# Optimization experiments

Measured on AMD Instinct MI355X. Metric: run time of the kernel, lower is better.

Reference implementation:

```python
import jax, jax.numpy as jnp
import numpy as np

N = 50000      # nodes
E = 800000     # raw edges (self-loops added inside reference, PyG GATConv default)
H = 8          # attention heads
DH = 16        # head dim
HID = H * DH   # 128 hidden
L = 4          # num GAT layers
G = 16         # graphs in the batch
EPS = 1e-5
NEG_SLOPE = 0.2


def setup_inputs() -> dict:
    key = jax.random.key(0)
    ks = jax.random.split(key, 8)
    s = 0.05
    x = jax.random.normal(ks[0], (N, 64), jnp.float32)
    edge_index = jax.random.randint(ks[1], (2, E), 0, N, dtype=jnp.int32).astype(jnp.int64)
    batch = jnp.sort(jax.random.randint(ks[2], (N,), 0, G, dtype=jnp.int32)).astype(jnp.int64)
    in_W = jax.random.normal(ks[3], (64, HID), jnp.float32) * s
    in_b = jnp.zeros((HID,), jnp.float32)
    Wg = jax.random.normal(ks[4], (L, HID, HID), jnp.float32) * s
    att_src = jax.random.normal(ks[5], (L, H, DH), jnp.float32) * s
    att_dst = jax.random.normal(ks[6], (L, H, DH), jnp.float32) * s
    gat_b = jnp.zeros((L, HID), jnp.float32)
    gn_w = jnp.ones((L, HID), jnp.float32)
    gn_b = jnp.zeros((L, HID), jnp.float32)
    gn_s = jnp.ones((L, HID), jnp.float32)  # GraphNorm mean_scale
    return {"x": x, "edge_index": edge_index, "batch": batch, "in_W": in_W,
            "in_b": in_b, "Wg": Wg, "att_src": att_src, "att_dst": att_dst,
            "gat_b": gat_b, "gn_w": gn_w, "gn_b": gn_b, "gn_s": gn_s}


def _gat_conv(h_in, src, dst, W, a_src, a_dst, bias):
    # PyG GATConv: per-head linear, additive attention, softmax over incoming edges
    h = (h_in @ W).reshape(N, H, DH)                       # [N,H,DH]
    e_src = jnp.sum(h * a_src, axis=-1)                    # [N,H]
    e_dst = jnp.sum(h * a_dst, axis=-1)                    # [N,H]
    e = jax.nn.leaky_relu(e_src[src] + e_dst[dst], NEG_SLOPE)  # [E',H]
    m = jax.ops.segment_max(e, dst, num_segments=N)        # per-dst max (stable softmax)
    m = jnp.where(jnp.isfinite(m), m, 0.0)
    ex = jnp.exp(e - m[dst])
    denom = jax.ops.segment_sum(ex, dst, num_segments=N)
    alpha = ex / (denom[dst] + 1e-16)                      # [E',H]
    msg = h[src] * alpha[..., None]                        # [E',H,DH]
    out = jax.ops.segment_sum(msg, dst, num_segments=N)    # [N,H,DH]
    return out.reshape(N, HID) + bias


def _graph_norm(x, batch, w, b, scale):
    cnt = jax.ops.segment_sum(jnp.ones((N, 1), x.dtype), batch, num_segments=G)
    mean = jax.ops.segment_sum(x, batch, num_segments=G) / cnt        # [G,HID]
    out = x - scale * mean[batch]
    var = jax.ops.segment_sum(out * out, batch, num_segments=G) / cnt # [G,HID]
    return out / jnp.sqrt(var + EPS)[batch] * w + b


def reference(x, edge_index, batch, in_W, in_b, Wg, att_src, att_dst, gat_b, gn_w, gn_b, gn_s):
    # add self-loops (PyG GATConv default add_self_loops=True)
    loop = jnp.arange(N, dtype=edge_index.dtype)
    src = jnp.concatenate([edge_index[0], loop])
    dst = jnp.concatenate([edge_index[1], loop])
    h = x @ in_W + in_b                                    # input_proj -> [N,HID]
    for i in range(L):
        attn = _gat_conv(h, src, dst, Wg[i], att_src[i], att_dst[i], gat_b[i])
        h = attn + h                                       # identity residual (in==out)
        h = _graph_norm(h, batch, gn_w[i], gn_b[i], gn_s[i])
        # dropout is identity in eval mode
    return h
```

## Files before the change

### kernel.cpp

```cpp
#include <hip/hip_runtime.h>
#include <cstdint>
#include <cstddef>

#define Nn   50000
#define Ee   800000
#define ETOT 850000
#define HID  128
#define Gg   16
#define RSZ  6250
#define NEG_SLOPE 0.2f
#define EPS_GN 1e-5f

typedef __attribute__((ext_vector_type(8))) short short8;
typedef __attribute__((ext_vector_type(4))) float f32x4;

static __device__ __forceinline__ float lrelu(float v) { return v > 0.f ? v : NEG_SLOPE * v; }

static __device__ __forceinline__ unsigned int f2bf(float x) {
    unsigned int u = __float_as_uint(x);
    return (u + 0x7fffu + ((u >> 16) & 1u)) >> 16;
}
static __device__ __forceinline__ float bf_lo(unsigned int u) { return __uint_as_float(u << 16); }
static __device__ __forceinline__ float bf_hi(unsigned int u) { return __uint_as_float(u & 0xffff0000u); }

__global__ void prep_w(const float* __restrict__ in_W, const float* __restrict__ Wg,
                       short* __restrict__ Wt0, short* __restrict__ Wtl) {
    int i = blockIdx.x * 256 + threadIdx.x;
    if (i < 8192) {
        int n = i >> 6, k = i & 63;
        Wt0[i] = (short)f2bf(in_W[k * 128 + n]);
    } else if (i < 73728) {
        int j = i - 8192;
        int l = j >> 14;
        int rkn = j & 16383;
        int n = rkn >> 7, k = rkn & 127;
        Wtl[j] = (short)f2bf(Wg[l * 16384 + k * 128 + n]);
    }
}

__global__ void count_deg(const int* __restrict__ edst, int* __restrict__ deg) {
    int r  = blockIdx.x & 7;
    int cb = blockIdx.x >> 3;
    int nb = gridDim.x >> 3;
    int lo = r * RSZ, hi = lo + RSZ;
    for (int i = cb * 256 + threadIdx.x; i < ETOT; i += nb * 256) {
        int dst = (i < Ee) ? edst[i] : (i - Ee);
        if (dst >= lo && dst < hi) atomicAdd(&deg[dst], 1);
    }
}

__global__ void scatter_edges(const int* __restrict__ esrc, const int* __restrict__ edst,
                              int* __restrict__ cur, int* __restrict__ col) {
    int r  = blockIdx.x & 7;
    int cb = blockIdx.x >> 3;
    int nb = gridDim.x >> 3;
    int lo = r * RSZ, hi = lo + RSZ;
    for (int i = cb * 256 + threadIdx.x; i < ETOT; i += nb * 256) {
        int dst = (i < Ee) ? edst[i] : (i - Ee);
        if (dst >= lo && dst < hi) {
            int src = (i < Ee) ? esrc[i] : dst;
            int pos = atomicAdd(&cur[dst], 1);
            col[pos] = src;
        }
    }
}

__global__ __launch_bounds__(1024) void scan1(const int* __restrict__ deg,
                                              int* __restrict__ rowptr,
                                              int* __restrict__ bsums) {
    __shared__ int sm[1024];
    int tid = threadIdx.x;
    int i = blockIdx.x * 1024 + tid;
    sm[tid] = (i < Nn) ? deg[i] : 0;
    __syncthreads();
    for (int off = 1; off < 1024; off <<= 1) {
        int t = 0;
        if (tid >= off) t = sm[tid - off];
        __syncthreads();
        sm[tid] += t;
        __syncthreads();
    }
    if (i < Nn) rowptr[i + 1] = sm[tid];
    if (tid == 1023) bsums[blockIdx.x] = sm[1023];
}

__global__ void scan2(int* __restrict__ bsums, int nb) {
    if (threadIdx.x == 0 && blockIdx.x == 0) {
        int run = 0;
        for (int b = 0; b < nb; b++) { int t = bsums[b]; bsums[b] = run; run += t; }
    }
}

__global__ void scan3(int* __restrict__ rowptr, const int* __restrict__ bsums) {
    int i = blockIdx.x * 256 + threadIdx.x;
    if (i == 0) rowptr[0] = 0;
    if (i < Nn) rowptr[i + 1] += bsums[i >> 10];
}

template <int K, bool AFFINE, bool OUT_BF16, bool BIAS>
__global__ __launch_bounds__(256) void gemm_mfma(const float* __restrict__ Ag,
                                                 const int* __restrict__ batch,
                                                 const float* __restrict__ Ab,
                                                 const float* __restrict__ Bb,
                                                 const short* __restrict__ Wt,
                                                 const float* __restrict__ bias,
                                                 float* __restrict__ Cf,
                                                 unsigned int* __restrict__ Cb,
                                                 int M) {
    constexpr int KP = K + 8;
    constexpr int ABYTES = 128 * KP * 2;
    constexpr int CBYTES = OUT_BF16 ? 64 * 130 * 4 : 0;
    constexpr int SBYTES = ABYTES > CBYTES ? ABYTES : CBYTES;
    __shared__ __align__(16) char smem[SBYTES];
    short* As = (short*)smem;
    float* Cs = (float*)smem;

    int t    = threadIdx.x;
    int lane = t & 63;
    int w    = t >> 6;
    int wm   = (w & 1) * 64;
    int wn   = (w >> 1) * 64;
    int row0 = blockIdx.x * 128;

    constexpr int F4R = K / 4;
    constexpr int ITERS = 128 * F4R / 256;
#pragma unroll
    for (int i = 0; i < ITERS; i++) {
        int f4 = t + 256 * i;
        int r  = f4 / F4R;
        int c4 = f4 % F4R;
        float4 v = make_float4(0.f, 0.f, 0.f, 0.f);
        int gr = row0 + r;
        if (gr < M) {
            v = *(const float4*)(Ag + (size_t)gr * K + c4 * 4);
            if (AFFINE) {
                int g = batch[gr];
                float4 Av = *(const float4*)(Ab + g * 128 + c4 * 4);
                float4 Bv = *(const float4*)(Bb + g * 128 + c4 * 4);
                v.x = v.x * Av.x + Bv.x;
                v.y = v.y * Av.y + Bv.y;
                v.z = v.z * Av.z + Bv.z;
                v.w = v.w * Av.w + Bv.w;
            }
        }
        uint2 pk;
        pk.x = f2bf(v.x) | (f2bf(v.y) << 16);
        pk.y = f2bf(v.z) | (f2bf(v.w) << 16);
        *(uint2*)(As + r * KP + c4 * 4) = pk;
    }
    __syncthreads();

    f32x4 acc[4][4] = {};
    int am = wm + (lane & 15);
    int aq = (lane >> 4) * 8;
    const short* wb = Wt + (size_t)(wn + (lane & 15)) * K + aq;
#pragma unroll
    for (int kk = 0; kk < K / 32; kk++) {
        short8 a[4], b[4];
#pragma unroll
        for (int nt = 0; nt < 4; nt++)
            b[nt] = *(const short8*)(wb + nt * 16 * K + kk * 32);
#pragma unroll
        for (int mt = 0; mt < 4; mt++)
            a[mt] = *(const short8*)(As + (am + mt * 16) * KP + kk * 32 + aq);
#pragma unroll
        for (int mt = 0; mt < 4; mt++)
#pragma unroll
            for (int nt = 0; nt < 4; nt++)
                acc[mt][nt] = __builtin_amdgcn_mfma_f32_16x16x32_bf16(
                    a[mt], b[nt], acc[mt][nt], 0, 0, 0);
    }

    if (!OUT_BF16) {
        float bv[4] = {0.f, 0.f, 0.f, 0.f};
        if (BIAS) {
#pragma unroll
            for (int nt = 0; nt < 4; nt++) bv[nt] = bias[wn + nt * 16 + (lane & 15)];
        }
#pragma unroll
        for (int mt = 0; mt < 4; mt++) {
#pragma unroll
            for (int reg = 0; reg < 4; reg++) {
                int row = row0 + wm + mt * 16 + (lane >> 4) * 4 + reg;
                if (row >= M) continue;
#pragma unroll
                for (int nt = 0; nt < 4; nt++)
                    Cf[(size_t)row * 128 + wn + nt * 16 + (lane & 15)] =
                        acc[mt][nt][reg] + bv[nt];
            }
        }
    } else {
#pragma unroll
        for (int half = 0; half < 2; half++) {
            __syncthreads();
            if ((w & 1) == half) {
#pragma unroll
                for (int mt = 0; mt < 4; mt++)
#pragma unroll
                    for (int reg = 0; reg < 4; reg++) {
                        int lr = mt * 16 + (lane >> 4) * 4 + reg;
#pragma unroll
                        for (int nt = 0; nt < 4; nt++)
                            Cs[lr * 130 + wn + nt * 16 + (lane & 15)] = acc[mt][nt][reg];
                    }
            }
            __syncthreads();
#pragma unroll
            for (int i = 0; i < 4; i++) {
                int u4 = t + 256 * i;
                int r  = u4 >> 4;
                int cu = (u4 & 15) * 4;
                int grow = row0 + half * 64 + r;
                if (grow < M) {
                    const float* cp = Cs + r * 130 + cu * 2;
                    float2 p0 = *(const float2*)(cp + 0);
                    float2 p1 = *(const float2*)(cp + 2);
                    float2 p2 = *(const float2*)(cp + 4);
                    float2 p3 = *(const float2*)(cp + 6);
                    uint4 o;
                    o.x = f2bf(p0.x) | (f2bf(p0.y) << 16);
                    o.y = f2bf(p1.x) | (f2bf(p1.y) << 16);
                    o.z = f2bf(p2.x) | (f2bf(p2.y) << 16);
                    o.w = f2bf(p3.x) | (f2bf(p3.y) << 16);
                    *(uint4*)(Cb + (size_t)grow * 64 + cu) = o;
                }
            }
        }
    }
}

__global__ __launch_bounds__(256) void att_scores(const unsigned int* __restrict__ hp,
                                                  const float* __restrict__ asrc,
                                                  const float* __restrict__ adst,
                                                  float* __restrict__ es,
                                                  float* __restrict__ ed) {
    int i = blockIdx.x * 256 + threadIdx.x;
    if (i >= Nn * 8) return;
    int hh = i & 7;
    const uint4* p = (const uint4*)(hp + (size_t)(i >> 3) * 64 + hh * 8);
    uint4 q0 = p[0], q1 = p[1];
    unsigned int qq[8] = {q0.x, q0.y, q0.z, q0.w, q1.x, q1.y, q1.z, q1.w};
    const float* av = asrc + hh * 16;
    const float* dv = adst + hh * 16;
    float s1 = 0.f, s2 = 0.f;
#pragma unroll
    for (int q = 0; q < 8; q++) {
        float x0 = bf_lo(qq[q]), x1 = bf_hi(qq[q]);
        s1 += x0 * av[2 * q] + x1 * av[2 * q + 1];
        s2 += x0 * dv[2 * q] + x1 * dv[2 * q + 1];
    }
    es[i] = s1;
    ed[i] = s2;
}

template <bool AFF>
__global__ __launch_bounds__(256) void gat_attn(const unsigned int* __restrict__ hp,
                                                const float* hin,
                                                const int* __restrict__ batch,
                                                const float* __restrict__ Ab,
                                                const float* __restrict__ Bb,
                                                const float* __restrict__ es,
                                                const float* __restrict__ ed,
                                                const int* __restrict__ rowptr,
                                                const int* __restrict__ col,
                                                const float* __restrict__ gbias,
                                                float* out) {
    int w    = threadIdx.x >> 6;
    int lane = threadIdx.x & 63;
    int n    = blockIdx.x * 4 + w;
    int start = rowptr[n], end = rowptr[n + 1];

    int slot = lane >> 3;
    int ah   = lane & 7;
    int ch   = lane >> 3;

    float edh = ed[(size_t)n * 8 + ah];

    float2 acc = make_float2(0.f, 0.f);
    float dacc = 0.f;

    int e0 = start;
    for (; e0 + 8 <= end; e0 += 8) {
        int src_l = col[e0 + slot];
        float wgt = __expf(lrelu(es[(size_t)src_l * 8 + ah] + edh));
        dacc += wgt;
#pragma unroll
        for (int j = 0; j < 8; j++) {
            int   src_j = __shfl(src_l, j * 8);
            float wj    = __shfl(wgt,   j * 8 + ch);
            unsigned int hv = hp[(size_t)src_j * 64 + lane];
            acc.x += wj * bf_lo(hv);
            acc.y += wj * bf_hi(hv);
        }
    }
    if (e0 < end) {
        int rem = end - e0;
        int eb  = e0 + slot;
        int ec  = (slot < rem) ? eb : (end - 1);
        int src_l = col[ec];
        float wgt = (slot < rem) ? __expf(lrelu(es[(size_t)src_l * 8 + ah] + edh)) : 0.f;
        dacc += wgt;
        for (int j = 0; j < rem; j++) {
            int   src_j = __shfl(src_l, j * 8);
            float wj    = __shfl(wgt,   j * 8 + ch);
            unsigned int hv = hp[(size_t)src_j * 64 + lane];
            acc.x += wj * bf_lo(hv);
            acc.y += wj * bf_hi(hv);
        }
    }

    dacc += __shfl_xor(dacc, 8);
    dacc += __shfl_xor(dacc, 16);
    dacc += __shfl_xor(dacc, 32);
    float inv  = 1.0f / (dacc + 1e-16f);
    float winv = __shfl(inv, ch);

    size_t idx = (size_t)n * 128 + 2 * lane;
    float2 xv = *(const float2*)(hin + idx);
    float2 res;
    if (AFF) {
        int g = batch[n];
        float2 Av = *(const float2*)(Ab + g * 128 + 2 * lane);
        float2 Bv = *(const float2*)(Bb + g * 128 + 2 * lane);
        res.x = xv.x * Av.x + Bv.x;
        res.y = xv.y * Av.y + Bv.y;
    } else {
        res = xv;
    }
    float2 o;
    o.x = acc.x * winv + gbias[2 * lane]     + res.x;
    o.y = acc.y * winv + gbias[2 * lane + 1] + res.y;
    *(float2*)(out + idx) = o;
}

#define SCHUNK 64
__global__ __launch_bounds__(128) void gn_stats(const float* __restrict__ x,
                                                const int* __restrict__ batch,
                                                float* __restrict__ sumx,
                                                float* __restrict__ sumxx,
                                                float* __restrict__ cnt) {
    int c  = threadIdx.x;
    int n0 = blockIdx.x * SCHUNK;
    int n1 = n0 + SCHUNK;
    if (n1 > Nn) n1 = Nn;
    if (n0 >= Nn) return;
    int curG = batch[n0];
    float sx = 0.f, sxx = 0.f;
    int run = 0;
    for (int n = n0; n < n1; n++) {
        int g = batch[n];
        if (g != curG) {
            atomicAdd(&sumx[curG * 128 + c], sx);
            atomicAdd(&sumxx[curG * 128 + c], sxx);
            if (c == 0) atomicAdd(&cnt[curG], (float)run);
            sx = 0.f; sxx = 0.f; run = 0; curG = g;
        }
        float v = x[(size_t)n * 128 + c];
        sx += v; sxx += v * v; run++;
    }
    atomicAdd(&sumx[curG * 128 + c], sx);
    atomicAdd(&sumxx[curG * 128 + c], sxx);
    if (c == 0) atomicAdd(&cnt[curG], (float)run);
}

__global__ void gn_final(const float* __restrict__ sumx, const float* __restrict__ sumxx,
                         const float* __restrict__ cnt, const float* __restrict__ w,
                         const float* __restrict__ b, const float* __restrict__ s,
                         float* __restrict__ Ab, float* __restrict__ Bb) {
    int i = blockIdx.x * blockDim.x + threadIdx.x;
    if (i >= Gg * 128) return;
    int g = i >> 7, c = i & 127;
    float cn  = cnt[g];
    float m   = sumx[i] / cn;
    float msq = sumxx[i] / cn;
    float sc  = s[c];
    float varo = msq - (2.f * sc - sc * sc) * m * m;
    float inv  = rsqrtf(varo + EPS_GN);
    float Ai   = inv * w[c];
    Ab[i] = Ai;
    Bb[i] = b[c] - sc * m * Ai;
    (void)g;
}

__global__ __launch_bounds__(256) void gn_apply(const float* __restrict__ x,
                                                const int* __restrict__ batch,
                                                const float* __restrict__ Ab,
                                                const float* __restrict__ Bb,
                                                float* __restrict__ out) {
    int idx = blockIdx.x * 256 + threadIdx.x;
    int n = idx >> 5;
    if (n >= Nn) return;
    int c4 = (idx & 31) << 2;
    int g = batch[n];
    float4 xv = *(const float4*)(x + (size_t)n * 128 + c4);
    float4 Av = *(const float4*)(Ab + g * 128 + c4);
    float4 Bv = *(const float4*)(Bb + g * 128 + c4);
    float4 o;
    o.x = xv.x * Av.x + Bv.x;
    o.y = xv.y * Av.y + Bv.y;
    o.z = xv.z * Av.z + Bv.z;
    o.w = xv.w * Av.w + Bv.w;
    *(float4*)(out + (size_t)n * 128 + c4) = o;
}

extern "C" void kernel_launch(void* const* d_in, const int* in_sizes, int n_in,
                              void* d_out, int out_size, void* d_ws, size_t ws_size,
                              hipStream_t stream) {
    const float* x      = (const float*)d_in[0];
    const int*   eidx   = (const int*)d_in[1];
    const int*   batch  = (const int*)d_in[2];
    const float* in_W   = (const float*)d_in[3];
    const float* in_b   = (const float*)d_in[4];
    const float* Wg     = (const float*)d_in[5];
    const float* attS   = (const float*)d_in[6];
    const float* attD   = (const float*)d_in[7];
    const float* gat_b  = (const float*)d_in[8];
    const float* gn_w   = (const float*)d_in[9];
    const float* gn_b   = (const float*)d_in[10];
    const float* gn_s   = (const float*)d_in[11];

    const int* esrc = eidx;
    const int* edst = eidx + Ee;

    char* p = (char*)d_ws;
    auto carve = [&](size_t bytes) {
        void* r = (void*)p;
        p += (bytes + 255) & ~(size_t)255;
        return r;
    };
    float* h0   = (float*)carve((size_t)Nn * 128 * 4);
    unsigned int* hp = (unsigned int*)carve((size_t)Nn * 64 * 4);
    float* h2   = (float*)carve((size_t)Nn * 128 * 4);
    float* es   = (float*)carve((size_t)Nn * 8 * 4);
    float* ed   = (float*)carve((size_t)Nn * 8 * 4);
    float* sumx = (float*)carve((size_t)(Gg * 128 * 2 + 16) * 4);
    float* sumxx = sumx + Gg * 128;
    float* cntf  = sumx + Gg * 128 * 2;
    float* Abuf = (float*)carve((size_t)Gg * 128 * 4);
    float* Bbuf = (float*)carve((size_t)Gg * 128 * 4);
    int* rowptr = (int*)carve((size_t)(Nn + 1) * 4);
    int* deg    = (int*)carve((size_t)Nn * 4);
    int* cur    = (int*)carve((size_t)Nn * 4);
    int* col    = (int*)carve((size_t)ETOT * 4);
    int* bsums  = (int*)carve(64 * 4);
    short* Wt0  = (short*)carve((size_t)128 * 64 * 2);
    short* Wtl  = (short*)carve((size_t)4 * 128 * 128 * 2);

    prep_w<<<288, 256, 0, stream>>>(in_W, Wg, Wt0, Wtl);
    hipMemsetAsync(deg, 0, (size_t)Nn * 4, stream);
    count_deg<<<768, 256, 0, stream>>>(edst, deg);
    scan1<<<(Nn + 1023) / 1024, 1024, 0, stream>>>(deg, rowptr, bsums);
    scan2<<<1, 64, 0, stream>>>(bsums, (Nn + 1023) / 1024);
    scan3<<<(Nn + 255) / 256, 256, 0, stream>>>(rowptr, bsums);
    hipMemcpyAsync(cur, rowptr, (size_t)Nn * 4, hipMemcpyDeviceToDevice, stream);
    scatter_edges<<<768, 256, 0, stream>>>(esrc, edst, cur, col);

    const int gemm_grid = (Nn + 127) / 128;

    gemm_mfma<64, false, false, true><<<gemm_grid, 256, 0, stream>>>(
        x, nullptr, nullptr, nullptr, Wt0, in_b, h0, nullptr, Nn);

    for (int l = 0; l < 4; l++) {
        const short* Wl = Wtl + (size_t)l * 128 * 128;
        if (l == 0) {
            gemm_mfma<128, false, true, false><<<gemm_grid, 256, 0, stream>>>(
                h0, nullptr, nullptr, nullptr, Wl, nullptr, nullptr, hp, Nn);
        } else {
            gemm_mfma<128, true, true, false><<<gemm_grid, 256, 0, stream>>>(
                h2, batch, Abuf, Bbuf, Wl, nullptr, nullptr, hp, Nn);
        }
        att_scores<<<(Nn * 8 + 255) / 256, 256, 0, stream>>>(hp, attS + l * 128,
                                                             attD + l * 128, es, ed);
        if (l == 0) {
            gat_attn<false><<<Nn / 4, 256, 0, stream>>>(hp, h0, nullptr, nullptr, nullptr,
                                                        es, ed, rowptr, col,
                                                        gat_b + l * 128, h2);
        } else {
            gat_attn<true><<<Nn / 4, 256, 0, stream>>>(hp, h2, batch, Abuf, Bbuf,
                                                       es, ed, rowptr, col,
                                                       gat_b + l * 128, h2);
        }
        hipMemsetAsync(sumx, 0, (size_t)(Gg * 128 * 2 + 16) * 4, stream);
        gn_stats<<<(Nn + SCHUNK - 1) / SCHUNK, 128, 0, stream>>>(h2, batch, sumx, sumxx, cntf);
        gn_final<<<8, 256, 0, stream>>>(sumx, sumxx, cntf, gn_w + l * 128,
                                        gn_b + l * 128, gn_s + l * 128, Abuf, Bbuf);
    }
    gn_apply<<<(Nn * 32 + 255) / 256, 256, 0, stream>>>(h2, batch, Abuf, Bbuf,
                                                        (float*)d_out);
    (void)in_sizes; (void)n_in; (void)out_size; (void)ws_size;
}
```

Baseline: 598.3 us.

## Fuse attention scores into GEMM epilogue and widen per-lane gathers in gat_attn

Drops the separate att_scores kernel and computes the per-head source and destination attention dot products in the bf16 GEMM epilogue, from the fp32 tile already held in shared memory. The scores now come from unrounded fp32 values rather than bf16-rounded ones. The aggregation kernel now has each half-wave handle alternate edges and each lane load 4 bf16 values (uint2), with a cross-half reduction at the end. The separate tail loop is removed by masking invalid edges to zero weight. This saves one launch and one re-read of hp per layer, but costs extra shuffles and some idle lanes in the final store.

Measured after the change: 575.9 us. -3.8%, faster.

```diff
diff --git a/kernel.cpp b/kernel.cpp
--- a/kernel.cpp
+++ b/kernel.cpp
@@ -97,13 +97,17 @@
     if (i < Nn) rowptr[i + 1] += bsums[i >> 10];
 }
 
-template <int K, bool AFFINE, bool OUT_BF16, bool BIAS>
+template <int K, bool AFFINE, bool OUT_BF16, bool BIAS, bool SCORES>
 __global__ __launch_bounds__(256) void gemm_mfma(const float* __restrict__ Ag,
                                                  const int* __restrict__ batch,
                                                  const float* __restrict__ Ab,
                                                  const float* __restrict__ Bb,
                                                  const short* __restrict__ Wt,
                                                  const float* __restrict__ bias,
+                                                 const float* __restrict__ asrc,
+                                                 const float* __restrict__ adst,
+                                                 float* __restrict__ es,
+                                                 float* __restrict__ ed,
                                                  float* __restrict__ Cf,
                                                  unsigned int* __restrict__ Cb,
                                                  int M) {
@@ -190,6 +194,15 @@
             }
         }
     } else {
+        float avv[8], dvv[8];
+        if (SCORES) {
+            int q = t & 15;
+#pragma unroll
+            for (int k = 0; k < 8; k++) {
+                avv[k] = asrc[q * 8 + k];
+                dvv[k] = adst[q * 8 + k];
+            }
+        }
 #pragma unroll
         for (int half = 0; half < 2; half++) {
             __syncthreads();
@@ -223,34 +236,25 @@
                     o.z = f2bf(p2.x) | (f2bf(p2.y) << 16);
                     o.w = f2bf(p3.x) | (f2bf(p3.y) << 16);
                     *(uint4*)(Cb + (size_t)grow * 64 + cu) = o;
+                    if (SCORES) {
+                        float s1 = p0.x * avv[0] + p0.y * avv[1] + p1.x * avv[2] +
+                                   p1.y * avv[3] + p2.x * avv[4] + p2.y * avv[5] +
+                                   p3.x * avv[6] + p3.y * avv[7];
+                        float s2 = p0.x * dvv[0] + p0.y * dvv[1] + p1.x * dvv[2] +
+                                   p1.y * dvv[3] + p2.x * dvv[4] + p2.y * dvv[5] +
+                                   p3.x * dvv[6] + p3.y * dvv[7];
+                        s1 += __shfl_xor(s1, 1);
+                        s2 += __shfl_xor(s2, 1);
+                        if ((t & 1) == 0) {
+                            int hh = (t & 15) >> 1;
+                            es[(size_t)grow * 8 + hh] = s1;
+                            ed[(size_t)grow * 8 + hh] = s2;
+                        }
+                    }
                 }
             }
         }
     }
-}
-
-__global__ __launch_bounds__(256) void att_scores(const unsigned int* __restrict__ hp,
-                                                  const float* __restrict__ asrc,
-                                                  const float* __restrict__ adst,
-                                                  float* __restrict__ es,
-                                                  float* __restrict__ ed) {
-    int i = blockIdx.x * 256 + threadIdx.x;
-    if (i >= Nn * 8) return;
-    int hh = i & 7;
-    const uint4* p = (const uint4*)(hp + (size_t)(i >> 3) * 64 + hh * 8);
-    uint4 q0 = p[0], q1 = p[1];
-    unsigned int qq[8] = {q0.x, q0.y, q0.z, q0.w, q1.x, q1.y, q1.z, q1.w};
-    const float* av = asrc + hh * 16;
-    const float* dv = adst + hh * 16;
-    float s1 = 0.f, s2 = 0.f;
-#pragma unroll
-    for (int q = 0; q < 8; q++) {
-        float x0 = bf_lo(qq[q]), x1 = bf_hi(qq[q]);
-        s1 += x0 * av[2 * q] + x1 * av[2 * q + 1];
-        s2 += x0 * dv[2 * q] + x1 * dv[2 * q + 1];
-    }
-    es[i] = s1;
-    ed[i] = s2;
 }
 
 template <bool AFF>
@@ -272,65 +276,70 @@
 
     int slot = lane >> 3;
     int ah   = lane & 7;
-    int ch   = lane >> 3;
+    int half = lane >> 5;
+    int sl   = lane & 31;
+    int hd   = sl >> 2;
 
     float edh = ed[(size_t)n * 8 + ah];
-
-    float2 acc = make_float2(0.f, 0.f);
+    const unsigned int* hpl = hp + sl * 2;
+
+    float a0 = 0.f, a1 = 0.f, a2 = 0.f, a3 = 0.f;
     float dacc = 0.f;
 
-    int e0 = start;
-    for (; e0 + 8 <= end; e0 += 8) {
-        int src_l = col[e0 + slot];
-        float wgt = __expf(lrelu(es[(size_t)src_l * 8 + ah] + edh));
+    for (int e0 = start; e0 < end; e0 += 8) {
+        int ee = e0 + slot;
+        bool valid = ee < end;
+        int ec = valid ? ee : (end - 1);
+        int src_l = col[ec];
+        float wgt = valid ? __expf(lrelu(es[(size_t)src_l * 8 + ah] + edh)) : 0.f;
         dacc += wgt;
 #pragma unroll
-        for (int j = 0; j < 8; j++) {
-            int   src_j = __shfl(src_l, j * 8);
-            float wj    = __shfl(wgt,   j * 8 + ch);
-            unsigned int hv = hp[(size_t)src_j * 64 + lane];
-            acc.x += wj * bf_lo(hv);
-            acc.y += wj * bf_hi(hv);
-        }
-    }
-    if (e0 < end) {
-        int rem = end - e0;
-        int eb  = e0 + slot;
-        int ec  = (slot < rem) ? eb : (end - 1);
-        int src_l = col[ec];
-        float wgt = (slot < rem) ? __expf(lrelu(es[(size_t)src_l * 8 + ah] + edh)) : 0.f;
-        dacc += wgt;
-        for (int j = 0; j < rem; j++) {
-            int   src_j = __shfl(src_l, j * 8);
-            float wj    = __shfl(wgt,   j * 8 + ch);
-            unsigned int hv = hp[(size_t)src_j * 64 + lane];
-            acc.x += wj * bf_lo(hv);
-            acc.y += wj * bf_hi(hv);
-        }
-    }
+        for (int jj = 0; jj < 4; jj++) {
+            int e = jj * 2 + half;
+            int   src_j = __shfl(src_l, e * 8);
+            float wj    = __shfl(wgt,   e * 8 + hd);
+            uint2 hv = *(const uint2*)(hpl + (size_t)src_j * 64);
+            a0 += wj * bf_lo(hv.x);
+            a1 += wj * bf_hi(hv.x);
+            a2 += wj * bf_lo(hv.y);
+            a3 += wj * bf_hi(hv.y);
+        }
+    }
+
+    a0 += __shfl_xor(a0, 32);
+    a1 += __shfl_xor(a1, 32);
+    a2 += __shfl_xor(a2, 32);
+    a3 += __shfl_xor(a3, 32);
 
     dacc += __shfl_xor(dacc, 8);
     dacc += __shfl_xor(dacc, 16);
     dacc += __shfl_xor(dacc, 32);
     float inv  = 1.0f / (dacc + 1e-16f);
-    float winv = __shfl(inv, ch);
-
-    size_t idx = (size_t)n * 128 + 2 * lane;
-    float2 xv = *(const float2*)(hin + idx);
-    float2 res;
-    if (AFF) {
-        int g = batch[n];
-        float2 Av = *(const float2*)(Ab + g * 128 + 2 * lane);
-        float2 Bv = *(const float2*)(Bb + g * 128 + 2 * lane);
-        res.x = xv.x * Av.x + Bv.x;
-        res.y = xv.y * Av.y + Bv.y;
-    } else {
-        res = xv;
-    }
-    float2 o;
-    o.x = acc.x * winv + gbias[2 * lane]     + res.x;
-    o.y = acc.y * winv + gbias[2 * lane + 1] + res.y;
-    *(float2*)(out + idx) = o;
+    float winv = __shfl(inv, hd);
+
+    if (half == 0) {
+        size_t idx = (size_t)n * 128 + sl * 4;
+        float4 xv = *(const float4*)(hin + idx);
+        float4 res;
+        if (AFF) {
+            int g = batch[n];
+            float4 Av = *(const float4*)(Ab + g * 128 + sl * 4);
+            float4 Bv = *(const float4*)(Bb + g * 128 + sl * 4);
+            res.x = xv.x * Av.x + Bv.x;
+            res.y = xv.y * Av.y + Bv.y;
+            res.z = xv.z * Av.z + Bv.z;
+            res.w = xv.w * Av.w + Bv.w;
+        } else {
+            res = xv;
+        }
+        float4 bv = *(const float4*)(gbias + sl * 4);
+        float4 o;
+        o.x = a0 * winv + bv.x + res.x;
+        o.y = a1 * winv + bv.y + res.y;
+        o.z = a2 * winv + bv.z + res.z;
+        o.w = a3 * winv + bv.w + res.w;
+        *(float4*)(out + idx) = o;
+    }
 }
 
 #define SCHUNK 64
@@ -457,20 +466,21 @@
 
     const int gemm_grid = (Nn + 127) / 128;
 
-    gemm_mfma<64, false, false, true><<<gemm_grid, 256, 0, stream>>>(
-        x, nullptr, nullptr, nullptr, Wt0, in_b, h0, nullptr, Nn);
+    gemm_mfma<64, false, false, true, false><<<gemm_grid, 256, 0, stream>>>(
+        x, nullptr, nullptr, nullptr, Wt0, in_b, nullptr, nullptr, nullptr, nullptr,
+        h0, nullptr, Nn);
 
     for (int l = 0; l < 4; l++) {
         const short* Wl = Wtl + (size_t)l * 128 * 128;
         if (l == 0) {
-            gemm_mfma<128, false, true, false><<<gemm_grid, 256, 0, stream>>>(
-                h0, nullptr, nullptr, nullptr, Wl, nullptr, nullptr, hp, Nn);
+            gemm_mfma<128, false, true, false, true><<<gemm_grid, 256, 0, stream>>>(
+                h0, nullptr, nullptr, nullptr, Wl, nullptr,
+                attS + l * 128, attD + l * 128, es, ed, nullptr, hp, Nn);
         } else {
-            gemm_mfma<128, true, true, false><<<gemm_grid, 256, 0, stream>>>(
-                h2, batch, Abuf, Bbuf, Wl, nullptr, nullptr, hp, Nn);
-        }
-        att_scores<<<(Nn * 8 + 255) / 256, 256, 0, stream>>>(hp, attS + l * 128,
-                                                             attD + l * 128, es, ed);
+            gemm_mfma<128, true, true, false, true><<<gemm_grid, 256, 0, stream>>>(
+                h2, batch, Abuf, Bbuf, Wl, nullptr,
+                attS + l * 128, attD + l * 128, es, ed, nullptr, hp, Nn);
+        }
         if (l == 0) {
             gat_attn<false><<<Nn / 4, 256, 0, stream>>>(hp, h0, nullptr, nullptr, nullptr,
                                                         es, ed, rowptr, col,
```
